# Kernel tuning notes

Hardware: AMD Instinct MI355X
Metric: run time of the kernel (lower is better)

## Reference

```python
import jax, jax.numpy as jnp
import numpy as np

WEIGHT_GT = 0.004
WEIGHT_BG = 0.0002
STRIDES = (8, 16, 32, 64, 128)
SIZES = (128, 64, 32, 16, 8)
B, C, N = 8, 256, 16


def setup_inputs() -> dict:
    key = jax.random.key(0)
    ks = jax.random.split(key, 32)
    inp = {}
    for i, hw in enumerate(SIZES):
        inp[f"feat_s{i}"] = jax.random.normal(ks[i], (B, C, hw, hw), jnp.float32)
        inp[f"feat_t{i}"] = jax.random.normal(ks[5 + i], (B, C, hw, hw), jnp.float32)
        inp[f"adapt_w{i}"] = jax.random.normal(ks[10 + i], (C, C), jnp.float32) * 0.05
        inp[f"adapt_b{i}"] = jnp.zeros((C,), jnp.float32)
    # valid boxes: x1<x2, y1<y2, inside a 1024px image
    x1 = jax.random.uniform(ks[20], (B, N), minval=0.0, maxval=800.0)
    y1 = jax.random.uniform(ks[21], (B, N), minval=0.0, maxval=800.0)
    bw = jax.random.uniform(ks[22], (B, N), minval=8.0, maxval=224.0)
    bh = jax.random.uniform(ks[23], (B, N), minval=8.0, maxval=224.0)
    inp["gt_bboxes"] = jnp.stack([x1, y1, x1 + bw, y1 + bh], axis=-1)  # [B,N,4]
    return inp


def gt_mask(gt_bboxes, h, w, stride):
    """Vectorized rasterization of the nested-loop mask builder. [B,N,4] -> [B,h,w]."""
    q = jnp.floor(gt_bboxes / stride).astype(jnp.int32)  # int() truncation (coords >= 0)
    lx = jnp.minimum(q[..., 0], w - 1)[:, :, None, None]  # [B,N,1,1]
    ly = jnp.minimum(q[..., 1], h - 1)[:, :, None, None]
    rx = jnp.minimum(q[..., 2], w - 1)[:, :, None, None]
    ry = jnp.minimum(q[..., 3], h - 1)[:, :, None, None]
    Y = jnp.arange(h)[:, None]  # [h,1]
    X = jnp.arange(w)[None, :]  # [1,w]
    degenerate = (lx == rx) | (ly == ry)
    inside = (Y >= ly) & (Y < ry) & (X >= lx) & (X < rx)   # slice ly:ry, lx:rx
    point = (Y == ly) & (X == lx)                          # single-pixel fallback
    per_box = jnp.where(degenerate, point, inside)         # [B,N,h,w]
    return jnp.any(per_box, axis=1).astype(jnp.float32)    # (mask > 0)


def _level_loss(feat_t, feat_s, w, b, gt_bboxes, stride):
    # 1x1-conv adaptation layer
    adapted = jnp.einsum('bchw,oc->bohw', feat_s, w) + b[None, :, None, None]
    h, wd = feat_t.shape[2], feat_t.shape[3]
    mask = gt_mask(gt_bboxes, h, wd, stride)[:, None, :, :]  # [B,1,H,W]
    diff = (feat_t - adapted) ** 2
    s_gt = jnp.sum(diff * mask)
    s_bg = jnp.sum(diff * (1.0 - mask))
    loss_gt = jnp.sqrt(s_gt + 1e-8)
    loss_bg = jnp.sqrt(s_bg + 1e-8)
    return WEIGHT_GT * loss_gt + WEIGHT_BG * loss_bg


def reference(feat_s0, feat_t0, adapt_w0, adapt_b0,
              feat_s1, feat_t1, adapt_w1, adapt_b1,
              feat_s2, feat_t2, adapt_w2, adapt_b2,
              feat_s3, feat_t3, adapt_w3, adapt_b3,
              feat_s4, feat_t4, adapt_w4, adapt_b4,
              gt_bboxes):
    fs = (feat_s0, feat_s1, feat_s2, feat_s3, feat_s4)
    ft = (feat_t0, feat_t1, feat_t2, feat_t3, feat_t4)
    ws = (adapt_w0, adapt_w1, adapt_w2, adapt_w3, adapt_w4)
    bs = (adapt_b0, adapt_b1, adapt_b2, adapt_b3, adapt_b4)
    loss = jnp.float32(0.0)
    for i in range(5):  # fixed, small number of pyramid levels
        loss = loss + _level_loss(ft[i], fs[i], ws[i], bs[i], gt_bboxes, STRIDES[i])
    return loss
```

## Files before the change

kernel.cpp:

```cpp
#include <hip/hip_runtime.h>
#include <math.h>

typedef __attribute__((ext_vector_type(8))) short short8;
typedef __attribute__((ext_vector_type(4))) float floatx4;

__device__ __forceinline__ short f2bf(float f) {
  union { float f; unsigned u; } v; v.f = f;
  unsigned r = v.u + 0x7fffu + ((v.u >> 16) & 1u);
  return (short)(r >> 16);
}

struct Params {
  const float* fs[5];
  const float* ft[5];
  const float* bias[5];
  const float* mask[5];
  const short8* wp[5];
  float* sums;
};

__global__ void prepack_w(const float* __restrict__ w0, const float* __restrict__ w1,
                          const float* __restrict__ w2, const float* __restrict__ w3,
                          const float* __restrict__ w4, short8* __restrict__ wp) {
  int id = blockIdx.x * 256 + threadIdx.x;
  if (id >= 5 * 8192) return;
  int lvl = id >> 13;
  int idx = id & 8191;
  const float* W = (lvl == 0) ? w0 : (lvl == 1) ? w1 : (lvl == 2) ? w2 : (lvl == 3) ? w3 : w4;
  int t16 = idx >> 9;
  int kt  = (idx >> 6) & 7;
  int ln  = idx & 63;
  int m = t16 * 16 + (ln & 15);
  int c = kt * 32 + (ln >> 4) * 8;
  const float* s = W + m * 256 + c;
  short8 v;
#pragma unroll
  for (int j = 0; j < 8; j++) v[j] = f2bf(s[j]);
  wp[id] = v;
}

__global__ void mask_kernel(const float* __restrict__ gtb, float* __restrict__ mask_base) {
  const int szs[5]  = {128, 64, 32, 16, 8};
  const int strd[5] = {8, 16, 32, 64, 128};
  const int offs[5] = {0, 131072, 163840, 172032, 174080};
  int b = blockIdx.x, lvl = blockIdx.y;
  int hw = szs[lvl];
  int P = hw * hw;
  __shared__ int lx[16], ly[16], rx[16], ry[16], dg[16];
  if (threadIdx.x < 16) {
    int n = threadIdx.x;
    const float* bb = gtb + (b * 16 + n) * 4;
    float inv = 1.0f / (float)strd[lvl];
    int qx1 = (int)floorf(bb[0] * inv);
    int qy1 = (int)floorf(bb[1] * inv);
    int qx2 = (int)floorf(bb[2] * inv);
    int qy2 = (int)floorf(bb[3] * inv);
    int wl = hw - 1;
    int a = min(qx1, wl), c = min(qy1, wl), d = min(qx2, wl), e = min(qy2, wl);
    lx[n] = a; ly[n] = c; rx[n] = d; ry[n] = e;
    dg[n] = (a == d) || (c == e);
  }
  __syncthreads();
  float* mp = mask_base + offs[lvl] + b * P;
  for (int p = threadIdx.x; p < P; p += blockDim.x) {
    int y = p / hw, x = p - y * hw;
    bool any = false;
#pragma unroll
    for (int n = 0; n < 16; n++) {
      bool cov = dg[n] ? (y == ly[n] && x == lx[n])
                       : (y >= ly[n] && y < ry[n] && x >= lx[n] && x < rx[n]);
      any = any || cov;
    }
    mp[p] = any ? 1.0f : 0.0f;
  }
}

template<int PL2, int LVL>
__device__ __forceinline__ void level_body(const Params& pr, int rem, float* red) {
  constexpr int P = 64 << PL2;
  const int tid  = threadIdx.x;
  const int lane = tid & 63;
  const int wave = tid >> 6;
  const int quad = lane >> 4, l15 = lane & 15;
  const int bz = rem >> PL2;
  const int p0 = (rem & ((1 << PL2) - 1)) << 6;

  const float*  fsb   = pr.fs[LVL]  + (size_t)bz * 256 * P;
  const float*  ftb   = pr.ft[LVL]  + (size_t)bz * 256 * P;
  const short8* wpb   = pr.wp[LVL]  + (size_t)wave * 4 * 8 * 64;
  const float*  maskb = pr.mask[LVL] + (size_t)bz * P;
  const float*  biasp = pr.bias[LVL];

  floatx4 acc[4][4];
#pragma unroll
  for (int i = 0; i < 4; i++)
#pragma unroll
    for (int j = 0; j < 4; j++) acc[i][j] = (floatx4){0.f, 0.f, 0.f, 0.f};

#pragma unroll 2
  for (int kt = 0; kt < 8; ++kt) {
    short8 af[4];
#pragma unroll
    for (int mi = 0; mi < 4; mi++)
      af[mi] = wpb[(mi * 8 + kt) * 64 + lane];

    short8 bf[4];
#pragma unroll
    for (int ni = 0; ni < 4; ni++) {
      const float* src = fsb + (size_t)(kt * 32 + quad * 8) * P + (p0 + ni * 16 + l15);
      float t[8];
#pragma unroll
      for (int j = 0; j < 8; j++) t[j] = src[(size_t)j * P];
      short8 v;
#pragma unroll
      for (int j = 0; j < 8; j++) v[j] = f2bf(t[j]);
      bf[ni] = v;
    }
#pragma unroll
    for (int mi = 0; mi < 4; mi++)
#pragma unroll
      for (int ni = 0; ni < 4; ni++)
        acc[mi][ni] = __builtin_amdgcn_mfma_f32_16x16x32_bf16(af[mi], bf[ni], acc[mi][ni], 0, 0, 0);
  }

  float sgt = 0.f, sbg = 0.f;
#pragma unroll
  for (int ni = 0; ni < 4; ni++) {
    int p = p0 + ni * 16 + l15;
    float mk = maskb[p];
#pragma unroll
    for (int mi = 0; mi < 4; mi++) {
      int ob = wave * 64 + mi * 16 + quad * 4;
      const float* ftp = ftb + (size_t)ob * P + p;
#pragma unroll
      for (int r = 0; r < 4; r++) {
        float ad = acc[mi][ni][r] + biasp[ob + r];
        float tv = ftp[(size_t)r * P];
        float d = tv - ad;
        float sq = d * d;
        sgt += sq * mk;
        sbg += sq - sq * mk;
      }
    }
  }
#pragma unroll
  for (int off = 32; off > 0; off >>= 1) {
    sgt += __shfl_down(sgt, off);
    sbg += __shfl_down(sbg, off);
  }
  if (lane == 0) { red[wave * 2] = sgt; red[wave * 2 + 1] = sbg; }
  __syncthreads();
  if (tid == 0) {
    atomicAdd(&pr.sums[LVL * 2 + 0], red[0] + red[2] + red[4] + red[6]);
    atomicAdd(&pr.sums[LVL * 2 + 1], red[1] + red[3] + red[5] + red[7]);
  }
}

__global__ __launch_bounds__(256, 2) void gemm_loss_all(Params pr) {
  __shared__ float red[8];
  int id = blockIdx.x;
  if (id < 2048)      level_body<8, 0>(pr, id,        red);
  else if (id < 2560) level_body<6, 1>(pr, id - 2048, red);
  else if (id < 2688) level_body<4, 2>(pr, id - 2560, red);
  else if (id < 2720) level_body<2, 3>(pr, id - 2688, red);
  else                level_body<0, 4>(pr, id - 2720, red);
}

__global__ void finalize(const float* __restrict__ sums, float* __restrict__ out) {
  if (threadIdx.x == 0 && blockIdx.x == 0) {
    float L = 0.f;
#pragma unroll
    for (int i = 0; i < 5; i++)
      L += 0.004f * sqrtf(sums[2 * i] + 1e-8f) + 0.0002f * sqrtf(sums[2 * i + 1] + 1e-8f);
    out[0] = L;
  }
}

extern "C" void kernel_launch(void* const* d_in, const int* in_sizes, int n_in,
                              void* d_out, int out_size, void* d_ws, size_t ws_size,
                              hipStream_t stream) {
  (void)in_sizes; (void)n_in; (void)out_size; (void)ws_size;
  const float* fs[5]; const float* ftp[5]; const float* aw[5]; const float* ab[5];
  for (int i = 0; i < 5; i++) {
    fs[i]  = (const float*)d_in[4 * i + 0];
    ftp[i] = (const float*)d_in[4 * i + 1];
    aw[i]  = (const float*)d_in[4 * i + 2];
    ab[i]  = (const float*)d_in[4 * i + 3];
  }
  const float* gtb = (const float*)d_in[20];
  float* out = (float*)d_out;
  char* ws = (char*)d_ws;

  float*  sums  = (float*)ws;
  float*  masks = (float*)(ws + 64);
  short8* wp    = (short8*)(ws + 64 + 698368);

  hipMemsetAsync(sums, 0, 64, stream);
  prepack_w<<<160, 256, 0, stream>>>(aw[0], aw[1], aw[2], aw[3], aw[4], wp);
  mask_kernel<<<dim3(8, 5), 256, 0, stream>>>(gtb, masks);

  const int moff[5] = {0, 131072, 163840, 172032, 174080};
  Params pr;
  for (int l = 0; l < 5; l++) {
    pr.fs[l]   = fs[l];
    pr.ft[l]   = ftp[l];
    pr.bias[l] = ab[l];
    pr.mask[l] = masks + moff[l];
    pr.wp[l]   = wp + l * 8192;
  }
  pr.sums = sums;

  gemm_loss_all<<<2728, 256, 0, stream>>>(pr);
  finalize<<<1, 64, 0, stream>>>(sums, out);
}
```

Baseline: 454.5 us.

## Stage student features through swizzled LDS with vectorized prefetch and fuse launches

Each block now issues all of its student-feature loads up front as float4 vector loads into registers. The data then goes through double-buffered, XOR-swizzled LDS, where lanes read the transposed B fragments instead of doing strided scalar global loads. The weight-prepack, mask and sum-zeroing kernels are merged into one launch, and the finalize kernel is replaced by a last-block-done atomic counter inside the GEMM kernel. This cuts uncoalesced global traffic and launch overhead, but adds 16 floatx4 registers per thread, a barrier on every k-step, and more LDS use, which may lower occupancy.

```diff
diff --git a/kernel.cpp b/kernel.cpp
--- a/kernel.cpp
+++ b/kernel.cpp
@@ -10,40 +10,48 @@
   return (short)(r >> 16);
 }
 
-struct Params {
+struct GParams {
   const float* fs[5];
   const float* ft[5];
   const float* bias[5];
   const float* mask[5];
   const short8* wp[5];
   float* sums;
+  float* out;
 };
 
-__global__ void prepack_w(const float* __restrict__ w0, const float* __restrict__ w1,
-                          const float* __restrict__ w2, const float* __restrict__ w3,
-                          const float* __restrict__ w4, short8* __restrict__ wp) {
-  int id = blockIdx.x * 256 + threadIdx.x;
-  if (id >= 5 * 8192) return;
-  int lvl = id >> 13;
-  int idx = id & 8191;
-  const float* W = (lvl == 0) ? w0 : (lvl == 1) ? w1 : (lvl == 2) ? w2 : (lvl == 3) ? w3 : w4;
-  int t16 = idx >> 9;
-  int kt  = (idx >> 6) & 7;
-  int ln  = idx & 63;
-  int m = t16 * 16 + (ln & 15);
-  int c = kt * 32 + (ln >> 4) * 8;
-  const float* s = W + m * 256 + c;
-  short8 v;
-#pragma unroll
-  for (int j = 0; j < 8; j++) v[j] = f2bf(s[j]);
-  wp[id] = v;
-}
-
-__global__ void mask_kernel(const float* __restrict__ gtb, float* __restrict__ mask_base) {
+__global__ void prep_all(const float* __restrict__ w0, const float* __restrict__ w1,
+                         const float* __restrict__ w2, const float* __restrict__ w3,
+                         const float* __restrict__ w4, const float* __restrict__ gtb,
+                         float* __restrict__ mask_base, short8* __restrict__ wp,
+                         float* __restrict__ sums) {
+  int bid = blockIdx.x;
+  if (bid == 200) {
+    if (threadIdx.x < 16) sums[threadIdx.x] = 0.f;
+    return;
+  }
+  if (bid < 160) {
+    int id = bid * 256 + threadIdx.x;
+    int lvl = id >> 13;
+    int idx = id & 8191;
+    const float* W = (lvl == 0) ? w0 : (lvl == 1) ? w1 : (lvl == 2) ? w2 : (lvl == 3) ? w3 : w4;
+    int t16 = idx >> 9;
+    int kt  = (idx >> 6) & 7;
+    int ln  = idx & 63;
+    int m = t16 * 16 + (ln & 15);
+    int c = kt * 32 + (ln >> 4) * 8;
+    const float* s = W + m * 256 + c;
+    short8 v;
+#pragma unroll
+    for (int j = 0; j < 8; j++) v[j] = f2bf(s[j]);
+    wp[id] = v;
+    return;
+  }
   const int szs[5]  = {128, 64, 32, 16, 8};
   const int strd[5] = {8, 16, 32, 64, 128};
   const int offs[5] = {0, 131072, 163840, 172032, 174080};
-  int b = blockIdx.x, lvl = blockIdx.y;
+  int id = bid - 160;
+  int b = id & 7, lvl = id >> 3;
   int hw = szs[lvl];
   int P = hw * hw;
   __shared__ int lx[16], ly[16], rx[16], ry[16], dg[16];
@@ -76,7 +84,7 @@
 }
 
 template<int PL2, int LVL>
-__device__ __forceinline__ void level_body(const Params& pr, int rem, float* red) {
+__device__ __forceinline__ void level_body(const GParams& pr, int rem, float* lds) {
   constexpr int P = 64 << PL2;
   const int tid  = threadIdx.x;
   const int lane = tid & 63;
@@ -85,42 +93,66 @@
   const int bz = rem >> PL2;
   const int p0 = (rem & ((1 << PL2) - 1)) << 6;
 
-  const float*  fsb   = pr.fs[LVL]  + (size_t)bz * 256 * P;
-  const float*  ftb   = pr.ft[LVL]  + (size_t)bz * 256 * P;
-  const short8* wpb   = pr.wp[LVL]  + (size_t)wave * 4 * 8 * 64;
+  const float*  fsb   = pr.fs[LVL] + (size_t)bz * 256 * P + p0;
+  const float*  ftb   = pr.ft[LVL] + (size_t)bz * 256 * P;
+  const short8* wpb   = pr.wp[LVL] + wave * 4 * 8 * 64;
   const float*  maskb = pr.mask[LVL] + (size_t)bz * P;
   const float*  biasp = pr.bias[LVL];
 
+  float* buf0 = lds;
+  float* buf1 = lds + 2048;
+  float* red  = lds + 4096;
+
+  const int fA = tid * 2,  cA = fA >> 4, pA = (fA & 15) << 2;
+  const int fB = fA + 1,   cB = fB >> 4, pB = (fB & 15) << 2;
+  floatx4 fr[16];
+#pragma unroll
+  for (int kt = 0; kt < 8; kt++) {
+    fr[kt * 2]     = *(const floatx4*)(fsb + (size_t)(kt * 32 + cA) * P + pA);
+    fr[kt * 2 + 1] = *(const floatx4*)(fsb + (size_t)(kt * 32 + cB) * P + pB);
+  }
+  const int swA = cA * 64 + (pA ^ ((cA >> 3) << 4));
+  const int swB = cB * 64 + (pB ^ ((cB >> 3) << 4));
+
   floatx4 acc[4][4];
 #pragma unroll
   for (int i = 0; i < 4; i++)
 #pragma unroll
     for (int j = 0; j < 4; j++) acc[i][j] = (floatx4){0.f, 0.f, 0.f, 0.f};
 
-#pragma unroll 2
-  for (int kt = 0; kt < 8; ++kt) {
+  *(floatx4*)(buf0 + swA) = fr[0];
+  *(floatx4*)(buf0 + swB) = fr[1];
+  __syncthreads();
+
+#pragma unroll
+  for (int kt = 0; kt < 8; kt++) {
+    float* rb = (kt & 1) ? buf1 : buf0;
+    float* wb = (kt & 1) ? buf0 : buf1;
+    if (kt < 7) {
+      *(floatx4*)(wb + swA) = fr[(kt + 1) * 2];
+      *(floatx4*)(wb + swB) = fr[(kt + 1) * 2 + 1];
+    }
     short8 af[4];
 #pragma unroll
+    for (int mi = 0; mi < 4; mi++) af[mi] = wpb[(mi * 8 + kt) * 64 + lane];
+
+    short8 bfr[4];
+#pragma unroll
+    for (int ni = 0; ni < 4; ni++) {
+      short8 v;
+#pragma unroll
+      for (int j = 0; j < 8; j++) {
+        float x = rb[(quad * 8 + j) * 64 + ((ni * 16 + l15) ^ (quad << 4))];
+        v[j] = f2bf(x);
+      }
+      bfr[ni] = v;
+    }
+#pragma unroll
     for (int mi = 0; mi < 4; mi++)
-      af[mi] = wpb[(mi * 8 + kt) * 64 + lane];
-
-    short8 bf[4];
-#pragma unroll
-    for (int ni = 0; ni < 4; ni++) {
-      const float* src = fsb + (size_t)(kt * 32 + quad * 8) * P + (p0 + ni * 16 + l15);
-      float t[8];
-#pragma unroll
-      for (int j = 0; j < 8; j++) t[j] = src[(size_t)j * P];
-      short8 v;
-#pragma unroll
-      for (int j = 0; j < 8; j++) v[j] = f2bf(t[j]);
-      bf[ni] = v;
-    }
-#pragma unroll
-    for (int mi = 0; mi < 4; mi++)
 #pragma unroll
       for (int ni = 0; ni < 4; ni++)
-        acc[mi][ni] = __builtin_amdgcn_mfma_f32_16x16x32_bf16(af[mi], bf[ni], acc[mi][ni], 0, 0, 0);
+        acc[mi][ni] = __builtin_amdgcn_mfma_f32_16x16x32_bf16(af[mi], bfr[ni], acc[mi][ni], 0, 0, 0);
+    __syncthreads();
   }
 
   float sgt = 0.f, sbg = 0.f;
@@ -153,27 +185,29 @@
   if (tid == 0) {
     atomicAdd(&pr.sums[LVL * 2 + 0], red[0] + red[2] + red[4] + red[6]);
     atomicAdd(&pr.sums[LVL * 2 + 1], red[1] + red[3] + red[5] + red[7]);
-  }
-}
-
-__global__ __launch_bounds__(256, 2) void gemm_loss_all(Params pr) {
-  __shared__ float red[8];
+    __threadfence();
+    unsigned old = atomicAdd((unsigned int*)(pr.sums + 12), 1u);
+    if (old == 2727u) {
+      float L = 0.f;
+#pragma unroll
+      for (int i = 0; i < 5; i++) {
+        float a = atomicAdd(&pr.sums[2 * i + 0], 0.f);
+        float b = atomicAdd(&pr.sums[2 * i + 1], 0.f);
+        L += 0.004f * sqrtf(a + 1e-8f) + 0.0002f * sqrtf(b + 1e-8f);
+      }
+      pr.out[0] = L;
+    }
+  }
+}
+
+__global__ __launch_bounds__(256, 2) void gemm_loss_all(GParams pr) {
+  __shared__ float lds[4096 + 16];
   int id = blockIdx.x;
-  if (id < 2048)      level_body<8, 0>(pr, id,        red);
-  else if (id < 2560) level_body<6, 1>(pr, id - 2048, red);
-  else if (id < 2688) level_body<4, 2>(pr, id - 2560, red);
-  else if (id < 2720) level_body<2, 3>(pr, id - 2688, red);
-  else                level_body<0, 4>(pr, id - 2720, red);
-}
-
-__global__ void finalize(const float* __restrict__ sums, float* __restrict__ out) {
-  if (threadIdx.x == 0 && blockIdx.x == 0) {
-    float L = 0.f;
-#pragma unroll
-    for (int i = 0; i < 5; i++)
-      L += 0.004f * sqrtf(sums[2 * i] + 1e-8f) + 0.0002f * sqrtf(sums[2 * i + 1] + 1e-8f);
-    out[0] = L;
-  }
+  if (id < 2048)      level_body<8, 0>(pr, id,        lds);
+  else if (id < 2560) level_body<6, 1>(pr, id - 2048, lds);
+  else if (id < 2688) level_body<4, 2>(pr, id - 2560, lds);
+  else if (id < 2720) level_body<2, 3>(pr, id - 2688, lds);
+  else                level_body<0, 4>(pr, id - 2720, lds);
 }
 
 extern "C" void kernel_launch(void* const* d_in, const int* in_sizes, int n_in,
@@ -195,12 +229,10 @@
   float*  masks = (float*)(ws + 64);
   short8* wp    = (short8*)(ws + 64 + 698368);
 
-  hipMemsetAsync(sums, 0, 64, stream);
-  prepack_w<<<160, 256, 0, stream>>>(aw[0], aw[1], aw[2], aw[3], aw[4], wp);
-  mask_kernel<<<dim3(8, 5), 256, 0, stream>>>(gtb, masks);
+  prep_all<<<201, 256, 0, stream>>>(aw[0], aw[1], aw[2], aw[3], aw[4], gtb, masks, wp, sums);
 
   const int moff[5] = {0, 131072, 163840, 172032, 174080};
-  Params pr;
+  GParams pr;
   for (int l = 0; l < 5; l++) {
     pr.fs[l]   = fs[l];
     pr.ft[l]   = ftp[l];
@@ -209,7 +241,7 @@
     pr.wp[l]   = wp + l * 8192;
   }
   pr.sums = sums;
+  pr.out  = out;
 
   gemm_loss_all<<<2728, 256, 0, stream>>>(pr);
-  finalize<<<1, 64, 0, stream>>>(sums, out);
-}
+}
```

Measured after the change: 567.3 us. +24.8%, slower.
